# Optimization experiments

Hardware: AMD Instinct MI355X
Metric: run time of the kernel (lower is better)

The kernel has to match this reference:

```python
import jax, jax.numpy as jnp
import numpy as np

N = 50000   # nodes
E = 1600000 # edges
D = 128     # feature dim (in = hidden = 128)


def setup_inputs() -> dict:
    key = jax.random.key(0)
    k1, k2, k3, k4 = jax.random.split(key, 4)
    scale = 1.0 / np.sqrt(D)
    return {
        "x": jax.random.normal(k1, (N, D), jnp.float32),
        "edge_index": jax.random.randint(k2, (2, E), 0, N, dtype=jnp.int32),
        "W0": jax.random.normal(k3, (D, D), jnp.float32) * scale,
        "b0": jnp.zeros((D,), jnp.float32),
        "W1": jax.random.normal(k4, (D, D), jnp.float32) * scale,
        "b1": jnp.zeros((D,), jnp.float32),
    }


def _gcn_norm(edge_index, num_nodes):
    # Add self-loops, compute symmetric normalization D^-1/2 A_hat D^-1/2.
    loop = jnp.arange(num_nodes, dtype=edge_index.dtype)
    src = jnp.concatenate([edge_index[0], loop])
    dst = jnp.concatenate([edge_index[1], loop])
    deg = jax.ops.segment_sum(jnp.ones_like(dst, jnp.float32), dst,
                              num_segments=num_nodes)
    dinv = jnp.where(deg > 0, jax.lax.rsqrt(deg), 0.0)
    norm = dinv[dst] * dinv[src]  # [E+N]
    return src, dst, norm


def _gcn_layer(x, src, dst, norm, W, b, num_nodes):
    h = x @ W                                  # [N, D]
    msg = h[src] * norm[:, None]               # gather + scale  [E+N, D]
    out = jax.ops.segment_sum(msg, dst, num_segments=num_nodes)  # scatter-add
    return out + b


def reference(x, edge_index, W0, b0, W1, b1):
    num_nodes = x.shape[0]
    src, dst, norm = _gcn_norm(edge_index, num_nodes)
    # forward loops over the first k=2 convs, ReLU after each (as in source)
    x = jax.nn.relu(_gcn_layer(x, src, dst, norm, W0, b0, num_nodes))
    x = jax.nn.relu(_gcn_layer(x, src, dst, norm, W1, b1, num_nodes))
    return x
```

## Files before the change

kernel.cpp:

```cpp
#include <hip/hip_runtime.h>
#include <hip/hip_bf16.h>

#define D 128
#define CHUNK 8192


typedef __attribute__((ext_vector_type(8))) short short8;
typedef __attribute__((ext_vector_type(4))) float floatx4;

static __device__ inline unsigned int f2bf(float f) {
    unsigned int u = __float_as_uint(f);
    return (u + 0x7FFFu + ((u >> 16) & 1u)) >> 16;
}
static __device__ inline float bflo(unsigned int u) { return __uint_as_float(u << 16); }
static __device__ inline float bfhi(unsigned int u) { return __uint_as_float(u & 0xFFFF0000u); }

__global__ __launch_bounds__(256) void k01_swz_hist(const float* __restrict__ W0,
                                                    const float* __restrict__ W1,
                                                    short8* __restrict__ whi0, short8* __restrict__ wlo0,
                                                    short8* __restrict__ whi1, short8* __restrict__ wlo1,
                                                    const int* __restrict__ dst,
                                                    int* __restrict__ blockhist, int E_) {
    __shared__ int h[256];
    const int tid = threadIdx.x;
    if (blockIdx.x < 16) {
        int gid = blockIdx.x * 256 + tid;
        const float* W = (gid < 2048) ? W0 : W1;
        short8* whi = (gid < 2048) ? whi0 : whi1;
        short8* wlo = (gid < 2048) ? wlo0 : wlo1;
        int t2 = gid & 2047;
        int t = t2 >> 8, q = (t2 >> 6) & 3, lane = t2 & 63;
        short8 hi, lo;
        #pragma unroll
        for (int j = 0; j < 8; ++j) {
            int k = q * 32 + (lane >> 4) * 8 + j;
            int n = t * 16 + (lane & 15);
            float w = W[k * D + n];
            unsigned int hh = f2bf(w);
            hi[j] = (short)hh;
            lo[j] = (short)f2bf(w - __uint_as_float(hh << 16));
        }
        whi[t2] = hi;
        wlo[t2] = lo;
    } else {
        const int b = blockIdx.x - 16;
        h[tid] = 0;
        __syncthreads();
        const int e0 = b * CHUNK;
        const int e1 = min(E_, e0 + CHUNK);
        for (int e = e0 + tid; e < e1; e += 256)
            atomicAdd(&h[dst[e] >> 8], 1);
        __syncthreads();
        blockhist[b * 256 + tid] = h[tid];
    }
}

__global__ __launch_bounds__(256) void k2_scan(const int* __restrict__ blockhist,
                                               int* __restrict__ gbase,
                                               int* __restrict__ bucket_offs,
                                               int NB, int NBUK, int E_) {
    __shared__ int s[256];
    const int tid = threadIdx.x;
    int run = 0;
    for (int c = 0; c < NB; ++c) {
        int t = blockhist[c * 256 + tid];
        gbase[c * 256 + tid] = run;
        run += t;
    }
    s[tid] = run;
    __syncthreads();
    #pragma unroll
    for (int off = 1; off < 256; off <<= 1) {
        int x = (tid >= off) ? s[tid - off] : 0;
        __syncthreads();
        s[tid] += x;
        __syncthreads();
    }
    int excl = s[tid] - run;
    if (tid < NBUK) bucket_offs[tid] = excl;
    if (tid == 0) bucket_offs[NBUK] = E_;
}

__global__ __launch_bounds__(256) void k3_scatter(const int* __restrict__ dst,
                                                  const int* __restrict__ src,
                                                  const int* __restrict__ gbase,
                                                  const int* __restrict__ bucket_offs,
                                                  unsigned int* __restrict__ buf, int E_, int NBUK) {
    __shared__ int c[256];
    const int b = blockIdx.x, tid = threadIdx.x;
    c[tid] = gbase[b * 256 + tid] + ((tid < NBUK) ? bucket_offs[tid] : 0);
    __syncthreads();
    const int e0 = b * CHUNK;
    const int e1 = min(E_, e0 + CHUNK);
    for (int e = e0 + tid; e < e1; e += 256) {
        int v = dst[e];
        int sdx = src[e];
        int pos = atomicAdd(&c[v >> 8], 1);
        buf[pos] = (unsigned int)sdx | ((unsigned int)(v & 255) << 16);
    }
}

__global__ __launch_bounds__(256) void k4_bucket(const unsigned int* __restrict__ buf,
                                                 const int* __restrict__ bucket_offs,
                                                 int* __restrict__ offs,
                                                 float* __restrict__ dinv,
                                                 int* __restrict__ col, int N_, int E_) {
    __shared__ int h[256];
    __shared__ int s[256];
    __shared__ int c[256];
    const int beta = blockIdx.x, tid = threadIdx.x;
    const int start = bucket_offs[beta];
    const int end   = bucket_offs[beta + 1];

    h[tid] = 0;
    __syncthreads();
    for (int e = start + tid; e < end; e += 256)
        atomicAdd(&h[(buf[e] >> 16) & 255], 1);
    __syncthreads();

    int deg = h[tid];
    s[tid] = deg;
    __syncthreads();
    #pragma unroll
    for (int off = 1; off < 256; off <<= 1) {
        int x = (tid >= off) ? s[tid - off] : 0;
        __syncthreads();
        s[tid] += x;
        __syncthreads();
    }
    int excl = s[tid] - deg;

    int v0 = beta * 256 + tid;
    if (v0 < N_) {
        offs[v0] = start + excl;
        dinv[v0] = rsqrtf((float)(deg + 1));
    }
    if (beta == 0 && tid == 0) offs[N_] = E_;
    c[tid] = start + excl;
    __syncthreads();

    for (int e = start + tid; e < end; e += 256) {
        unsigned int p = buf[e];
        int pos = atomicAdd(&c[(p >> 16) & 255], 1);
        col[pos] = (int)(p & 0xFFFFu);
    }
}

__global__ __launch_bounds__(256) void gemm_mfma(const float* __restrict__ A,
                                                 const short8* __restrict__ whi,
                                                 const short8* __restrict__ wlo,
                                                 const float* __restrict__ dinv,
                                                 unsigned int* __restrict__ Gu, int nrows) {
    __shared__ float tileT[128][65];

    const int tid  = threadIdx.x;
    const int wave = tid >> 6, lane = tid & 63;
    const int m = lane & 15, quad = lane >> 4;
    const int rowInBlk = wave * 16;
    const int arow = min(blockIdx.x * 64 + rowInBlk + m, nrows - 1);
    const float* Ap = A + (size_t)arow * D + quad * 8;

    floatx4 acc[8];
    #pragma unroll
    for (int t = 0; t < 8; ++t) acc[t] = (floatx4){0.f, 0.f, 0.f, 0.f};

    #pragma unroll
    for (int q = 0; q < 4; ++q) {
        float4 a0 = *(const float4*)(Ap + q * 32);
        float4 a1 = *(const float4*)(Ap + q * 32 + 4);
        float av[8] = {a0.x, a0.y, a0.z, a0.w, a1.x, a1.y, a1.z, a1.w};
        short8 ahi, alo;
        #pragma unroll
        for (int j = 0; j < 8; ++j) {
            unsigned int h = f2bf(av[j]);
            ahi[j] = (short)h;
            alo[j] = (short)f2bf(av[j] - __uint_as_float(h << 16));
        }
        #pragma unroll
        for (int t = 0; t < 8; ++t) {
            short8 bh = whi[(t * 4 + q) * 64 + lane];
            short8 bl = wlo[(t * 4 + q) * 64 + lane];
            acc[t] = __builtin_amdgcn_mfma_f32_16x16x32_bf16(ahi, bh, acc[t], 0, 0, 0);
            acc[t] = __builtin_amdgcn_mfma_f32_16x16x32_bf16(alo, bh, acc[t], 0, 0, 0);
            acc[t] = __builtin_amdgcn_mfma_f32_16x16x32_bf16(ahi, bl, acc[t], 0, 0, 0);
        }
    }

    #pragma unroll
    for (int t = 0; t < 8; ++t)
        #pragma unroll
        for (int r = 0; r < 4; ++r)
            tileT[t * 16 + m][rowInBlk + quad * 4 + r] = acc[t][r];
    __syncthreads();

    const int orow = tid >> 2, seg = tid & 3;
    const int grow = blockIdx.x * 64 + orow;
    if (grow < nrows) {
        float s = dinv[grow];
        const int p = seg >> 1;
        unsigned int* Gp = Gu + ((size_t)(p * nrows + grow)) * 32 + (seg & 1) * 16;
        #pragma unroll
        for (int i = 0; i < 4; ++i) {
            int c0 = seg * 32 + i * 8;
            uint4 o4;
            o4.x = f2bf(tileT[c0 + 0][orow] * s) | (f2bf(tileT[c0 + 1][orow] * s) << 16);
            o4.y = f2bf(tileT[c0 + 2][orow] * s) | (f2bf(tileT[c0 + 3][orow] * s) << 16);
            o4.z = f2bf(tileT[c0 + 4][orow] * s) | (f2bf(tileT[c0 + 5][orow] * s) << 16);
            o4.w = f2bf(tileT[c0 + 6][orow] * s) | (f2bf(tileT[c0 + 7][orow] * s) << 16);
            ((uint4*)Gp)[i] = o4;
        }
    }
}

__global__ __launch_bounds__(256) void aggregate_kernel(const unsigned int* __restrict__ Gu,
                                                        const int* __restrict__ offs,
                                                        const int* __restrict__ col,
                                                        const float* __restrict__ dinv,
                                                        const float* __restrict__ bias,
                                                        float* __restrict__ out, int nnodes) {
    const int lane  = threadIdx.x & 31;
    const int node  = blockIdx.x * 8 + (threadIdx.x >> 5);
    const int plane = blockIdx.y;
    if (node >= nnodes) return;
    const unsigned int* P = Gu + (size_t)plane * nnodes * 32;

    unsigned int su = P[(size_t)node * 32 + lane];
    float ax = bflo(su), ay = bfhi(su);

    int s = offs[node];
    int e = offs[node + 1];
    int idx = s;
    for (; idx + 8 <= e; idx += 8) {
        int j0 = col[idx + 0], j1 = col[idx + 1], j2 = col[idx + 2], j3 = col[idx + 3];
        int j4 = col[idx + 4], j5 = col[idx + 5], j6 = col[idx + 6], j7 = col[idx + 7];
        unsigned int u0 = P[(size_t)j0 * 32 + lane];
        unsigned int u1 = P[(size_t)j1 * 32 + lane];
        unsigned int u2 = P[(size_t)j2 * 32 + lane];
        unsigned int u3 = P[(size_t)j3 * 32 + lane];
        unsigned int u4 = P[(size_t)j4 * 32 + lane];
        unsigned int u5 = P[(size_t)j5 * 32 + lane];
        unsigned int u6 = P[(size_t)j6 * 32 + lane];
        unsigned int u7 = P[(size_t)j7 * 32 + lane];
        ax += ((bflo(u0) + bflo(u1)) + (bflo(u2) + bflo(u3))) +
              ((bflo(u4) + bflo(u5)) + (bflo(u6) + bflo(u7)));
        ay += ((bfhi(u0) + bfhi(u1)) + (bfhi(u2) + bfhi(u3))) +
              ((bfhi(u4) + bfhi(u5)) + (bfhi(u6) + bfhi(u7)));
    }
    for (; idx + 4 <= e; idx += 4) {
        int j0 = col[idx + 0], j1 = col[idx + 1], j2 = col[idx + 2], j3 = col[idx + 3];
        unsigned int u0 = P[(size_t)j0 * 32 + lane];
        unsigned int u1 = P[(size_t)j1 * 32 + lane];
        unsigned int u2 = P[(size_t)j2 * 32 + lane];
        unsigned int u3 = P[(size_t)j3 * 32 + lane];
        ax += (bflo(u0) + bflo(u1)) + (bflo(u2) + bflo(u3));
        ay += (bfhi(u0) + bfhi(u1)) + (bfhi(u2) + bfhi(u3));
    }
    for (; idx < e; ++idx) {
        unsigned int u = P[(size_t)col[idx] * 32 + lane];
        ax += bflo(u);
        ay += bfhi(u);
    }

    float dv = dinv[node];
    float2 bb = ((const float2*)bias)[plane * 32 + lane];
    float2 o;
    o.x = fmaxf(fmaf(dv, ax, bb.x), 0.f);
    o.y = fmaxf(fmaf(dv, ay, bb.y), 0.f);
    ((float2*)out)[(size_t)node * 64 + plane * 32 + lane] = o;
}

extern "C" void kernel_launch(void* const* d_in, const int* in_sizes, int n_in,
                              void* d_out, int out_size, void* d_ws, size_t ws_size,
                              hipStream_t stream) {
    const float* x    = (const float*)d_in[0];
    const int*   edge = (const int*)d_in[1];
    const float* W0   = (const float*)d_in[2];
    const float* b0   = (const float*)d_in[3];
    const float* W1   = (const float*)d_in[4];
    const float* b1   = (const float*)d_in[5];
    float* out = (float*)d_out;

    const int N_ = in_sizes[0] / D;
    const int E_ = in_sizes[1] / 2;
    const int* srcp = edge;
    const int* dstp = edge + E_;

    const int NB   = (E_ + CHUNK - 1) / CHUNK;
    const int NBUK = (N_ + 255) >> 8;

    char* p = (char*)d_ws;
    auto carve = [&](size_t bytes) { char* q = p; p += (bytes + 255) & ~(size_t)255; return q; };
    int*          blockhist = (int*)          carve((size_t)NB * 256 * 4);
    int*          gbase     = (int*)          carve((size_t)NB * 256 * 4);
    int*          buck_offs = (int*)          carve((size_t)(NBUK + 1) * 4);
    int*          offs      = (int*)          carve((size_t)(N_ + 1) * 4);
    float*        dinv      = (float*)        carve((size_t)N_ * 4);
    unsigned int* buf       = (unsigned int*) carve((size_t)E_ * 4);
    int*          col       = (int*)          carve((size_t)E_ * 4);
    unsigned int* gu        = (unsigned int*) carve((size_t)N_ * 64 * 4);
    short8*       whi0      = (short8*)       carve(2048 * 16);
    short8*       wlo0      = (short8*)       carve(2048 * 16);
    short8*       whi1      = (short8*)       carve(2048 * 16);
    short8*       wlo1      = (short8*)       carve(2048 * 16);

    k01_swz_hist<<<16 + NB, 256, 0, stream>>>(W0, W1, whi0, wlo0, whi1, wlo1,
                                              dstp, blockhist, E_);
    k2_scan     <<<1,       256, 0, stream>>>(blockhist, gbase, buck_offs, NB, NBUK, E_);
    k3_scatter  <<<NB,      256, 0, stream>>>(dstp, srcp, gbase, buck_offs, buf, E_, NBUK);
    k4_bucket   <<<NBUK,    256, 0, stream>>>(buf, buck_offs, offs, dinv, col, N_, E_);

    const int gmb = (N_ + 63) / 64;
    dim3 ab((N_ + 7) / 8, 2);

    gemm_mfma       <<<gmb, 256, 0, stream>>>(x, whi0, wlo0, dinv, gu, N_);
    aggregate_kernel<<<ab,  256, 0, stream>>>(gu, offs, col, dinv, b0, out, N_);
    gemm_mfma       <<<gmb, 256, 0, stream>>>(out, whi1, wlo1, dinv, gu, N_);
    aggregate_kernel<<<ab,  256, 0, stream>>>(gu, offs, col, dinv, b1, out, N_);
}
```

Measured before the change: 307.1 us.

## Parallelize bucket scan across blocks and pin aggregate planes to XCD halves

The single-block serial scan over per-chunk histograms is replaced by one block per chunk. Each block recomputes the column totals and its own prefix, then writes its global base directly, so the scatter kernel no longer adds bucket offsets. The aggregate kernel's 2D grid is flattened and remapped so blocks of each feature plane land on a fixed half of the XCDs (block id mod 8). This is meant to keep each plane's gathered rows resident in those XCDs' L2 caches. The trade-off is that every scan block redundantly reads the whole histogram.

```diff
diff --git a/kernel.cpp b/kernel.cpp
--- a/kernel.cpp
+++ b/kernel.cpp
@@ -60,14 +60,15 @@
                                                int* __restrict__ bucket_offs,
                                                int NB, int NBUK, int E_) {
     __shared__ int s[256];
-    const int tid = threadIdx.x;
-    int run = 0;
-    for (int c = 0; c < NB; ++c) {
-        int t = blockhist[c * 256 + tid];
-        gbase[c * 256 + tid] = run;
-        run += t;
-    }
-    s[tid] = run;
+    const int myb = blockIdx.x, tid = threadIdx.x;
+    int total = 0, prefix = 0;
+    #pragma unroll 4
+    for (int b2 = 0; b2 < NB; ++b2) {
+        int t = blockhist[b2 * 256 + tid];
+        total += t;
+        prefix += (b2 < myb) ? t : 0;
+    }
+    s[tid] = total;
     __syncthreads();
     #pragma unroll
     for (int off = 1; off < 256; off <<= 1) {
@@ -76,19 +77,21 @@
         s[tid] += x;
         __syncthreads();
     }
-    int excl = s[tid] - run;
-    if (tid < NBUK) bucket_offs[tid] = excl;
-    if (tid == 0) bucket_offs[NBUK] = E_;
+    int bstart = s[tid] - total;
+    gbase[myb * 256 + tid] = bstart + prefix;
+    if (myb == 0) {
+        if (tid < NBUK) bucket_offs[tid] = bstart;
+        if (tid == 0) bucket_offs[NBUK] = E_;
+    }
 }
 
 __global__ __launch_bounds__(256) void k3_scatter(const int* __restrict__ dst,
                                                   const int* __restrict__ src,
                                                   const int* __restrict__ gbase,
-                                                  const int* __restrict__ bucket_offs,
-                                                  unsigned int* __restrict__ buf, int E_, int NBUK) {
+                                                  unsigned int* __restrict__ buf, int E_) {
     __shared__ int c[256];
     const int b = blockIdx.x, tid = threadIdx.x;
-    c[tid] = gbase[b * 256 + tid] + ((tid < NBUK) ? bucket_offs[tid] : 0);
+    c[tid] = gbase[b * 256 + tid];
     __syncthreads();
     const int e0 = b * CHUNK;
     const int e1 = min(E_, e0 + CHUNK);
@@ -217,10 +220,15 @@
                                                         const int* __restrict__ col,
                                                         const float* __restrict__ dinv,
                                                         const float* __restrict__ bias,
-                                                        float* __restrict__ out, int nnodes) {
-    const int lane  = threadIdx.x & 31;
-    const int node  = blockIdx.x * 8 + (threadIdx.x >> 5);
-    const int plane = blockIdx.y;
+                                                        float* __restrict__ out, int nnodes,
+                                                        int ngroups) {
+    const int bid  = blockIdx.x;
+    const int xcd  = bid & 7;
+    const int plane = xcd >> 2;
+    const int i    = (bid >> 3) * 4 + (xcd & 3);
+    if (i >= ngroups) return;
+    const int lane = threadIdx.x & 31;
+    const int node = i * 8 + (threadIdx.x >> 5);
     if (node >= nnodes) return;
     const unsigned int* P = Gu + (size_t)plane * nnodes * 32;
 
@@ -305,15 +313,16 @@
 
     k01_swz_hist<<<16 + NB, 256, 0, stream>>>(W0, W1, whi0, wlo0, whi1, wlo1,
                                               dstp, blockhist, E_);
-    k2_scan     <<<1,       256, 0, stream>>>(blockhist, gbase, buck_offs, NB, NBUK, E_);
-    k3_scatter  <<<NB,      256, 0, stream>>>(dstp, srcp, gbase, buck_offs, buf, E_, NBUK);
+    k2_scan     <<<NB,      256, 0, stream>>>(blockhist, gbase, buck_offs, NB, NBUK, E_);
+    k3_scatter  <<<NB,      256, 0, stream>>>(dstp, srcp, gbase, buf, E_);
     k4_bucket   <<<NBUK,    256, 0, stream>>>(buf, buck_offs, offs, dinv, col, N_, E_);
 
     const int gmb = (N_ + 63) / 64;
-    dim3 ab((N_ + 7) / 8, 2);
-
-    gemm_mfma       <<<gmb, 256, 0, stream>>>(x, whi0, wlo0, dinv, gu, N_);
-    aggregate_kernel<<<ab,  256, 0, stream>>>(gu, offs, col, dinv, b0, out, N_);
-    gemm_mfma       <<<gmb, 256, 0, stream>>>(out, whi1, wlo1, dinv, gu, N_);
-    aggregate_kernel<<<ab,  256, 0, stream>>>(gu, offs, col, dinv, b1, out, N_);
-}
+    const int ngroups = (N_ + 7) / 8;
+    const int agrid   = ((ngroups + 3) / 4) * 8;
+
+    gemm_mfma       <<<gmb,   256, 0, stream>>>(x, whi0, wlo0, dinv, gu, N_);
+    aggregate_kernel<<<agrid, 256, 0, stream>>>(gu, offs, col, dinv, b0, out, N_, ngroups);
+    gemm_mfma       <<<gmb,   256, 0, stream>>>(out, whi1, wlo1, dinv, gu, N_);
+    aggregate_kernel<<<agrid, 256, 0, stream>>>(gu, offs, col, dinv, b1, out, N_, ngroups);
+}
```

Measured after the change: 269.1 us. 1.14x faster.
